# Optimization experiments

Hardware: AMD Instinct MI355X
Metric: run time of the kernel (lower is better)

## Reference

```python
import jax, jax.numpy as jnp
import numpy as np
import math

FACTOR = 1

def setup_inputs() -> dict:
    key = jax.random.key(0)
    k1, k2, k3 = jax.random.split(key, 3)
    B, L, H, E = 32, 1024, 8, 64
    return {
        "queries": jax.random.normal(k1, (B, L, H, E), dtype=jnp.float32),
        "keys": jax.random.normal(k2, (B, L, H, E), dtype=jnp.float32),
        "values": jax.random.normal(k3, (B, L, H, E), dtype=jnp.float32),
        "attn_mask": 0,
    }


def reference(queries, keys, values, attn_mask):
    # queries/keys/values: [B, L, H, E] (S == L so no pad/truncate needed)
    B, L, H, E = queries.shape
    q = jnp.transpose(queries, (0, 2, 3, 1))  # [B,H,E,L]
    k = jnp.transpose(keys, (0, 2, 3, 1))
    v = jnp.transpose(values, (0, 2, 3, 1))   # [B,H,D,L]

    # FFT cross-correlation
    q_fft = jnp.fft.rfft(q, axis=-1)
    k_fft = jnp.fft.rfft(k, axis=-1)
    corr = jnp.fft.irfft(q_fft * jnp.conj(k_fft), n=L, axis=-1)  # [B,H,E,L]

    # top-k delay selection (global over batch, as in source)
    top_k = min(int(FACTOR * math.log(L)), L // 4, 32)  # static: 6
    mean_value = corr.mean(axis=(1, 2))                 # [B,L]
    weights, indices = jax.lax.top_k(mean_value.mean(axis=0), top_k)  # [k]
    tmp_corr = jax.nn.softmax(weights)                  # [k]

    # weighted circular-shift aggregation: roll(v, -indices[i]) summed with tmp_corr[i]
    pos = (jnp.arange(L)[None, :] + indices[:, None]) % L  # [k,L]
    patterns = v[:, :, :, pos]                              # [B,H,D,k,L]
    delays_agg = jnp.einsum('k,bhdkl->bhdl', tmp_corr, patterns)

    return jnp.transpose(delays_agg, (0, 3, 1, 2))  # [B,L,H,D]
```

## Files before the change

kernel.cpp:

```cpp
#include <hip/hip_runtime.h>
#include <math.h>

#define L_SEQ 1024
#define TOPK 6
#define SSTR 1057
#define NFBLK 2048

__device__ constexpr float TW32R[16] = {
  1.f, 0.98078528f, 0.92387953f, 0.83146961f, 0.70710678f, 0.55557023f,
  0.38268343f, 0.19509032f, 0.f, -0.19509032f, -0.38268343f, -0.55557023f,
  -0.70710678f, -0.83146961f, -0.92387953f, -0.98078528f};
__device__ constexpr float TW32I[16] = {
  0.f, -0.19509032f, -0.38268343f, -0.55557023f, -0.70710678f, -0.83146961f,
  -0.92387953f, -0.98078528f, -1.f, -0.98078528f, -0.92387953f, -0.83146961f,
  -0.70710678f, -0.55557023f, -0.38268343f, -0.19509032f};

#define FFTSTAGE(M, H, SH)                                                \
  _Pragma("unroll")                                                       \
  for (int k_ = 0; k_ < 32; k_ += (M)) {                                  \
    _Pragma("unroll")                                                     \
    for (int t_ = 0; t_ < (H); ++t_) {                                    \
      const int a_ = k_ + t_, b_ = a_ + (H);                              \
      const int m_ = t_ << (SH);                                          \
      float vr_, vi_;                                                     \
      if (m_ == 0)      { vr_ = zr[b_]; vi_ = zi[b_]; }                   \
      else if (m_ == 8) { vr_ = zi[b_]; vi_ = -zr[b_]; }                  \
      else {                                                              \
        vr_ = zr[b_] * TW32R[m_] - zi[b_] * TW32I[m_];                    \
        vi_ = zr[b_] * TW32I[m_] + zi[b_] * TW32R[m_];                    \
      }                                                                   \
      zr[b_] = zr[a_] - vr_; zi[b_] = zi[a_] - vi_;                       \
      zr[a_] += vr_;         zi[a_] += vi_;                               \
    }                                                                     \
  }

__global__ __launch_bounds__(256, 2) void fft_spec_kernel(
    const float* __restrict__ q, const float* __restrict__ k,
    float* __restrict__ partial)
{
  __shared__ float smem[8 * SSTR];

  const int tid = threadIdx.x;
  const int bid = blockIdx.x;

  const int wq  = bid >> 3;
  const int xcd = bid & 7;
  const int octet = (wq & 1) | (((wq >> 1) & 3) << 1);
  const int h = (wq >> 3) & 7;
  const int b = (xcd << 2) | (wq >> 6);

  const float* qb = q + (size_t)b * 524288 + h * 64 + octet * 8;
  const float* kb = k + (size_t)b * 524288 + h * 64 + octet * 8;

  const int ep = (tid & 1) * 4;
  const int lb = tid >> 1;
  float4 qv[8], kv[8];
  int colv[8];
  #pragma unroll
  for (int it = 0; it < 8; ++it) {
    const int l = it * 128 + lb;
    qv[it] = *(const float4*)(qb + (size_t)l * 512 + ep);
    kv[it] = *(const float4*)(kb + (size_t)l * 512 + ep);
    colv[it] = (l & 31) * 33 + (l >> 5);
  }

  #pragma unroll
  for (int it = 0; it < 8; ++it) {
    const int col = colv[it];
    smem[(ep + 0) * SSTR + col] = qv[it].x;
    smem[(ep + 1) * SSTR + col] = qv[it].y;
    smem[(ep + 2) * SSTR + col] = qv[it].z;
    smem[(ep + 3) * SSTR + col] = qv[it].w;
  }
  __syncthreads();

  const int s = tid >> 5;
  const int i = tid & 31;
  constexpr int BR[32] = {0,16,8,24,4,20,12,28,2,18,10,26,6,22,14,30,
                          1,17,9,25,5,21,13,29,3,19,11,27,7,23,15,31};
  const float astep = (float)i * 6.13592315e-03f;
  const int rowbase = s * SSTR + i * 33;
  float zr[32], zi[32];

  #pragma unroll
  for (int c = 0; c < 32; ++c) zr[BR[c]] = smem[rowbase + c];
  __syncthreads();

  #pragma unroll
  for (int it = 0; it < 8; ++it) {
    const int col = colv[it];
    smem[(ep + 0) * SSTR + col] = kv[it].x;
    smem[(ep + 1) * SSTR + col] = kv[it].y;
    smem[(ep + 2) * SSTR + col] = kv[it].z;
    smem[(ep + 3) * SSTR + col] = kv[it].w;
  }
  __syncthreads();
  #pragma unroll
  for (int c = 0; c < 32; ++c) zi[BR[c]] = smem[rowbase + c];
  __syncthreads();

  FFTSTAGE(2, 1, 4) FFTSTAGE(4, 2, 3) FFTSTAGE(8, 4, 2)
  FFTSTAGE(16, 8, 1) FFTSTAGE(32, 16, 0)
  #pragma unroll
  for (int k2 = 1; k2 < 32; ++k2) {
    float sa, ca;
    __sincosf(astep * (float)k2, &sa, &ca);
    const float nr = zr[k2] * ca + zi[k2] * sa;
    const float ni = zi[k2] * ca - zr[k2] * sa;
    zr[k2] = nr; zi[k2] = ni;
  }

  const int j = i;
  #pragma unroll
  for (int k2 = 0; k2 < 32; ++k2) smem[rowbase + k2] = zr[k2];
  __syncthreads();
  #pragma unroll
  for (int c = 0; c < 32; ++c) zr[c] = smem[s * SSTR + BR[c] * 33 + j];
  __syncthreads();
  #pragma unroll
  for (int k2 = 0; k2 < 32; ++k2) smem[rowbase + k2] = zi[k2];
  __syncthreads();
  #pragma unroll
  for (int c = 0; c < 32; ++c) zi[c] = smem[s * SSTR + BR[c] * 33 + j];
  __syncthreads();

  FFTSTAGE(2, 1, 4) FFTSTAGE(4, 2, 3) FFTSTAGE(8, 4, 2)
  FFTSTAGE(16, 8, 1) FFTSTAGE(32, 16, 0)

  const int t64 = tid & 63;
  const int pl = (t64 & 32) | ((32 - j) & 31);
  const int rowS = s * SSTR + j * 33;
  float si_all[32];

  #pragma unroll
  for (int k1 = 0; k1 < 16; ++k1) {
    float xr = __shfl(zr[31 - k1], pl, 64);
    float xi = __shfl(zi[31 - k1], pl, 64);
    if (j == 0) { xr = zr[(32 - k1) & 31]; xi = zi[(32 - k1) & 31]; }
    const float ar = zr[k1], ai = zi[k1];
    smem[rowS + k1] = 0.5f  * (ar * xi + ai * xr);
    si_all[k1]      = 0.25f * (ar * ar + ai * ai - xr * xr - xi * xi);
  }
  #pragma unroll
  for (int k1 = 16; k1 < 32; ++k1) {
    float xr = __shfl(zr[31 - k1], pl, 64);
    float xi = __shfl(zi[31 - k1], pl, 64);
    if (j == 0) { xr = zr[(32 - k1) & 31]; xi = zi[(32 - k1) & 31]; }
    const float ar = zr[k1], ai = zi[k1];
    smem[rowS + k1] = 0.5f  * (ar * xi + ai * xr);
    si_all[k1]      = 0.25f * (ar * ar + ai * ai - xr * xr - xi * xi);
  }
  __syncthreads();

  const int jj = tid >> 3;
  const int kq = tid & 7;
  const int v = jj * 32 + kq * 4;
  {
    float ar4[4] = {0.f, 0.f, 0.f, 0.f};
    #pragma unroll
    for (int pp = 0; pp < 8; ++pp) {
      const int base = pp * SSTR + jj * 33 + kq * 4;
      #pragma unroll
      for (int m = 0; m < 4; ++m) ar4[m] += smem[base + m];
    }
    *(float4*)(partial + (size_t)bid * 2048 + v) =
        make_float4(ar4[0], ar4[1], ar4[2], ar4[3]);
  }
  __syncthreads();

  #pragma unroll
  for (int k1 = 0; k1 < 32; ++k1) smem[rowS + k1] = si_all[k1];
  __syncthreads();
  {
    float ai4[4] = {0.f, 0.f, 0.f, 0.f};
    #pragma unroll
    for (int pp = 0; pp < 8; ++pp) {
      const int base = pp * SSTR + jj * 33 + kq * 4;
      #pragma unroll
      for (int m = 0; m < 4; ++m) ai4[m] += smem[base + m];
    }
    *(float4*)(partial + (size_t)bid * 2048 + 1024 + v) =
        make_float4(ai4[0], ai4[1], ai4[2], ai4[3]);
  }
}

__global__ __launch_bounds__(256) void spec_reduce(
    const float* __restrict__ partial, float* __restrict__ S4)
{
  const int t = threadIdx.x;
  const int b64 = t & 63, rq = t >> 6;
  const int vb = (blockIdx.x & 31) * 64;
  const int rc = blockIdx.x >> 5;
  const int v = vb + b64;
  float acc = 0.f;
  const int r0 = rc * 512 + rq * 128;
  for (int rr = r0; rr < r0 + 128; ++rr)
    acc += partial[(size_t)rr * 2048 + v];
  __shared__ float sm[4][65];
  sm[rq][b64] = acc;
  __syncthreads();
  if (t < 64)
    S4[(size_t)rc * 2048 + vb + t] =
        sm[0][t] + sm[1][t] + sm[2][t] + sm[3][t];
}

__global__ __launch_bounds__(256) void corr_kernel(
    const float* __restrict__ S4, float* __restrict__ c)
{
  __shared__ float Sr[2048];
  __shared__ float sm[8][33];
  const int t = threadIdx.x;
  #pragma unroll
  for (int u = 0; u < 8; ++u) {
    const int v = u * 256 + t;
    Sr[v] = S4[v] + S4[2048 + v] + S4[4096 + v] + S4[6144 + v];
  }
  __syncthreads();

  const int tau = blockIdx.x * 32 + (t & 31);
  const int jc = t >> 5;
  float acc = 0.f;
  #pragma unroll 4
  for (int jj = 0; jj < 128; ++jj) {
    const int v = jc * 128 + jj;
    const int jt = ((v & 31) << 5) | (v >> 5);
    float s_, c_;
    __sincosf((float)((jt * tau) & 1023) * 6.13592315e-03f, &s_, &c_);
    acc += Sr[v] * c_ - Sr[1024 + v] * s_;
  }
  sm[jc][t & 31] = acc;
  __syncthreads();
  if (t < 32) {
    float r = 0.f;
    #pragma unroll
    for (int g = 0; g < 8; ++g) r += sm[g][t];
    c[blockIdx.x * 32 + t] = r * (1.0f / 16777216.0f);
  }
}

__global__ __launch_bounds__(256) void topk_kernel(
    const float* __restrict__ c, int* __restrict__ idx_out,
    float* __restrict__ w_out)
{
  __shared__ float vals[L_SEQ];
  __shared__ float rv[256];
  __shared__ int ri[256];
  __shared__ float topv[TOPK];
  __shared__ int topi[TOPK];
  const int tid = threadIdx.x;
  for (int i = tid; i < L_SEQ; i += 256) vals[i] = c[i];
  __syncthreads();

  for (int kk = 0; kk < TOPK; ++kk) {
    float bv = -INFINITY;
    int bi = 1 << 30;
    for (int i = tid; i < L_SEQ; i += 256) {
      const float v = vals[i];
      if (v > bv || (v == bv && i < bi)) { bv = v; bi = i; }
    }
    rv[tid] = bv; ri[tid] = bi;
    __syncthreads();
    for (int off = 128; off > 0; off >>= 1) {
      if (tid < off) {
        const float v2 = rv[tid + off];
        const int i2 = ri[tid + off];
        if (v2 > rv[tid] || (v2 == rv[tid] && i2 < ri[tid])) {
          rv[tid] = v2; ri[tid] = i2;
        }
      }
      __syncthreads();
    }
    if (tid == 0) {
      topv[kk] = rv[0];
      topi[kk] = ri[0];
      vals[ri[0]] = -INFINITY;
    }
    __syncthreads();
  }

  if (tid == 0) {
    const float m = topv[0];
    float e[TOPK], sum = 0.f;
    for (int i = 0; i < TOPK; ++i) { e[i] = expf(topv[i] - m); sum += e[i]; }
    const float inv = 1.0f / sum;
    for (int i = 0; i < TOPK; ++i) { w_out[i] = e[i] * inv; idx_out[i] = topi[i]; }
  }
}

__global__ __launch_bounds__(256) void agg_kernel(
    const float* __restrict__ v, const int* __restrict__ idx,
    const float* __restrict__ w, float4* __restrict__ out)
{
  __shared__ int sidx[TOPK];
  __shared__ float sw[TOPK];
  if (threadIdx.x < TOPK) {
    sidx[threadIdx.x] = idx[threadIdx.x];
    sw[threadIdx.x] = w[threadIdx.x];
  }
  __syncthreads();

  const int i = blockIdx.x * 256 + threadIdx.x;
  const int he4 = i & 127;
  const int l = (i >> 7) & (L_SEQ - 1);
  const int b = i >> 17;
  const float4* vb = (const float4*)v + (size_t)b * (L_SEQ * 128);

  float4 acc = make_float4(0.f, 0.f, 0.f, 0.f);
  #pragma unroll
  for (int kk = 0; kk < TOPK; ++kk) {
    const int src = (l + sidx[kk]) & (L_SEQ - 1);
    const float4 vv = vb[(size_t)src * 128 + he4];
    const float wk = sw[kk];
    acc.x += wk * vv.x; acc.y += wk * vv.y;
    acc.z += wk * vv.z; acc.w += wk * vv.w;
  }
  out[i] = acc;
}

extern "C" void kernel_launch(void* const* d_in, const int* in_sizes, int n_in,
                              void* d_out, int out_size, void* d_ws, size_t ws_size,
                              hipStream_t stream) {
  const float* q = (const float*)d_in[0];
  const float* k = (const float*)d_in[1];
  const float* v = (const float*)d_in[2];

  float* out = (float*)d_out;
  float* partial = out;
  float* S4 = out + (size_t)8388608;

  float* c    = (float*)d_ws;
  int*   idxp = (int*)((char*)d_ws + 4096);
  float* wp   = (float*)((char*)d_ws + 4096 + 64);

  fft_spec_kernel<<<NFBLK, 256, 0, stream>>>(q, k, partial);
  spec_reduce<<<128, 256, 0, stream>>>(partial, S4);
  corr_kernel<<<32, 256, 0, stream>>>(S4, c);
  topk_kernel<<<1, 256, 0, stream>>>(c, idxp, wp);
  agg_kernel<<<(L_SEQ * 32 * 128) / 256, 256, 0, stream>>>(v, idxp, wp,
                                                           (float4*)out);
}
```

Measured before the change: 131.4 us.

## Process two octets per FFT block and simplify spectrum reduction

Each fft_spec_kernel block now loops over two channel octets, accumulating spectra in registers, which halves the grid to 1024 blocks and halves the partial-sum buffer. spec_reduce becomes a single-level reduction over 1024 rows into one spectrum held in workspace, and corr_kernel reads it directly instead of summing four chunks. The aim is less partial traffic and smaller reduction work, at the cost of fewer blocks in flight and a serialized second pass without load/compute overlap.

```diff
diff --git a/kernel.cpp b/kernel.cpp
--- a/kernel.cpp
+++ b/kernel.cpp
@@ -4,7 +4,7 @@
 #define L_SEQ 1024
 #define TOPK 6
 #define SSTR 1057
-#define NFBLK 2048
+#define NFBLK 1024
 
 __device__ constexpr float TW32R[16] = {
   1.f, 0.98078528f, 0.92387953f, 0.83146961f, 0.70710678f, 0.55557023f,
@@ -45,34 +45,9 @@
 
   const int wq  = bid >> 3;
   const int xcd = bid & 7;
-  const int octet = (wq & 1) | (((wq >> 1) & 3) << 1);
-  const int h = (wq >> 3) & 7;
-  const int b = (xcd << 2) | (wq >> 6);
-
-  const float* qb = q + (size_t)b * 524288 + h * 64 + octet * 8;
-  const float* kb = k + (size_t)b * 524288 + h * 64 + octet * 8;
-
-  const int ep = (tid & 1) * 4;
-  const int lb = tid >> 1;
-  float4 qv[8], kv[8];
-  int colv[8];
-  #pragma unroll
-  for (int it = 0; it < 8; ++it) {
-    const int l = it * 128 + lb;
-    qv[it] = *(const float4*)(qb + (size_t)l * 512 + ep);
-    kv[it] = *(const float4*)(kb + (size_t)l * 512 + ep);
-    colv[it] = (l & 31) * 33 + (l >> 5);
-  }
-
-  #pragma unroll
-  for (int it = 0; it < 8; ++it) {
-    const int col = colv[it];
-    smem[(ep + 0) * SSTR + col] = qv[it].x;
-    smem[(ep + 1) * SSTR + col] = qv[it].y;
-    smem[(ep + 2) * SSTR + col] = qv[it].z;
-    smem[(ep + 3) * SSTR + col] = qv[it].w;
-  }
-  __syncthreads();
+  const int op  = wq & 3;
+  const int h   = (wq >> 2) & 7;
+  const int b   = (xcd << 2) | (wq >> 5);
 
   const int s = tid >> 5;
   const int i = tid & 31;
@@ -80,132 +55,158 @@
                           1,17,9,25,5,21,13,29,3,19,11,27,7,23,15,31};
   const float astep = (float)i * 6.13592315e-03f;
   const int rowbase = s * SSTR + i * 33;
-  float zr[32], zi[32];
-
-  #pragma unroll
-  for (int c = 0; c < 32; ++c) zr[BR[c]] = smem[rowbase + c];
-  __syncthreads();
-
-  #pragma unroll
-  for (int it = 0; it < 8; ++it) {
-    const int col = colv[it];
-    smem[(ep + 0) * SSTR + col] = kv[it].x;
-    smem[(ep + 1) * SSTR + col] = kv[it].y;
-    smem[(ep + 2) * SSTR + col] = kv[it].z;
-    smem[(ep + 3) * SSTR + col] = kv[it].w;
-  }
-  __syncthreads();
-  #pragma unroll
-  for (int c = 0; c < 32; ++c) zi[BR[c]] = smem[rowbase + c];
-  __syncthreads();
-
-  FFTSTAGE(2, 1, 4) FFTSTAGE(4, 2, 3) FFTSTAGE(8, 4, 2)
-  FFTSTAGE(16, 8, 1) FFTSTAGE(32, 16, 0)
-  #pragma unroll
-  for (int k2 = 1; k2 < 32; ++k2) {
-    float sa, ca;
-    __sincosf(astep * (float)k2, &sa, &ca);
-    const float nr = zr[k2] * ca + zi[k2] * sa;
-    const float ni = zi[k2] * ca - zr[k2] * sa;
-    zr[k2] = nr; zi[k2] = ni;
-  }
-
-  const int j = i;
-  #pragma unroll
-  for (int k2 = 0; k2 < 32; ++k2) smem[rowbase + k2] = zr[k2];
-  __syncthreads();
-  #pragma unroll
-  for (int c = 0; c < 32; ++c) zr[c] = smem[s * SSTR + BR[c] * 33 + j];
-  __syncthreads();
-  #pragma unroll
-  for (int k2 = 0; k2 < 32; ++k2) smem[rowbase + k2] = zi[k2];
-  __syncthreads();
-  #pragma unroll
-  for (int c = 0; c < 32; ++c) zi[c] = smem[s * SSTR + BR[c] * 33 + j];
-  __syncthreads();
-
-  FFTSTAGE(2, 1, 4) FFTSTAGE(4, 2, 3) FFTSTAGE(8, 4, 2)
-  FFTSTAGE(16, 8, 1) FFTSTAGE(32, 16, 0)
-
-  const int t64 = tid & 63;
-  const int pl = (t64 & 32) | ((32 - j) & 31);
-  const int rowS = s * SSTR + j * 33;
-  float si_all[32];
-
-  #pragma unroll
-  for (int k1 = 0; k1 < 16; ++k1) {
-    float xr = __shfl(zr[31 - k1], pl, 64);
-    float xi = __shfl(zi[31 - k1], pl, 64);
-    if (j == 0) { xr = zr[(32 - k1) & 31]; xi = zi[(32 - k1) & 31]; }
-    const float ar = zr[k1], ai = zi[k1];
-    smem[rowS + k1] = 0.5f  * (ar * xi + ai * xr);
-    si_all[k1]      = 0.25f * (ar * ar + ai * ai - xr * xr - xi * xi);
-  }
-  #pragma unroll
-  for (int k1 = 16; k1 < 32; ++k1) {
-    float xr = __shfl(zr[31 - k1], pl, 64);
-    float xi = __shfl(zi[31 - k1], pl, 64);
-    if (j == 0) { xr = zr[(32 - k1) & 31]; xi = zi[(32 - k1) & 31]; }
-    const float ar = zr[k1], ai = zi[k1];
-    smem[rowS + k1] = 0.5f  * (ar * xi + ai * xr);
-    si_all[k1]      = 0.25f * (ar * ar + ai * ai - xr * xr - xi * xi);
-  }
-  __syncthreads();
+  const int ep = (tid & 1) * 4;
+  const int lb = tid >> 1;
 
   const int jj = tid >> 3;
   const int kq = tid & 7;
-  const int v = jj * 32 + kq * 4;
-  {
-    float ar4[4] = {0.f, 0.f, 0.f, 0.f};
+  float ar4[4] = {0.f, 0.f, 0.f, 0.f};
+  float ai4[4] = {0.f, 0.f, 0.f, 0.f};
+
+  for (int oc = 0; oc < 2; ++oc) {
+    const int octet = op * 2 + oc;
+    const float* qb = q + (size_t)b * 524288 + h * 64 + octet * 8;
+    const float* kb = k + (size_t)b * 524288 + h * 64 + octet * 8;
+
+    if (oc) __syncthreads();
+
+    float4 qv[8], kv[8];
+    int colv[8];
+    #pragma unroll
+    for (int it = 0; it < 8; ++it) {
+      const int l = it * 128 + lb;
+      qv[it] = *(const float4*)(qb + (size_t)l * 512 + ep);
+      kv[it] = *(const float4*)(kb + (size_t)l * 512 + ep);
+      colv[it] = (l & 31) * 33 + (l >> 5);
+    }
+
+    #pragma unroll
+    for (int it = 0; it < 8; ++it) {
+      const int col = colv[it];
+      smem[(ep + 0) * SSTR + col] = qv[it].x;
+      smem[(ep + 1) * SSTR + col] = qv[it].y;
+      smem[(ep + 2) * SSTR + col] = qv[it].z;
+      smem[(ep + 3) * SSTR + col] = qv[it].w;
+    }
+    __syncthreads();
+
+    float zr[32], zi[32];
+    #pragma unroll
+    for (int c = 0; c < 32; ++c) zr[BR[c]] = smem[rowbase + c];
+    __syncthreads();
+
+    #pragma unroll
+    for (int it = 0; it < 8; ++it) {
+      const int col = colv[it];
+      smem[(ep + 0) * SSTR + col] = kv[it].x;
+      smem[(ep + 1) * SSTR + col] = kv[it].y;
+      smem[(ep + 2) * SSTR + col] = kv[it].z;
+      smem[(ep + 3) * SSTR + col] = kv[it].w;
+    }
+    __syncthreads();
+    #pragma unroll
+    for (int c = 0; c < 32; ++c) zi[BR[c]] = smem[rowbase + c];
+    __syncthreads();
+
+    FFTSTAGE(2, 1, 4) FFTSTAGE(4, 2, 3) FFTSTAGE(8, 4, 2)
+    FFTSTAGE(16, 8, 1) FFTSTAGE(32, 16, 0)
+    #pragma unroll
+    for (int k2 = 1; k2 < 32; ++k2) {
+      float sa, ca;
+      __sincosf(astep * (float)k2, &sa, &ca);
+      const float nr = zr[k2] * ca + zi[k2] * sa;
+      const float ni = zi[k2] * ca - zr[k2] * sa;
+      zr[k2] = nr; zi[k2] = ni;
+    }
+
+    const int j = i;
+    #pragma unroll
+    for (int k2 = 0; k2 < 32; ++k2) smem[rowbase + k2] = zr[k2];
+    __syncthreads();
+    #pragma unroll
+    for (int c = 0; c < 32; ++c) zr[c] = smem[s * SSTR + BR[c] * 33 + j];
+    __syncthreads();
+    #pragma unroll
+    for (int k2 = 0; k2 < 32; ++k2) smem[rowbase + k2] = zi[k2];
+    __syncthreads();
+    #pragma unroll
+    for (int c = 0; c < 32; ++c) zi[c] = smem[s * SSTR + BR[c] * 33 + j];
+    __syncthreads();
+
+    FFTSTAGE(2, 1, 4) FFTSTAGE(4, 2, 3) FFTSTAGE(8, 4, 2)
+    FFTSTAGE(16, 8, 1) FFTSTAGE(32, 16, 0)
+
+    const int t64 = tid & 63;
+    const int pl = (t64 & 32) | ((32 - j) & 31);
+    const int rowS = s * SSTR + j * 33;
+    float si_all[32];
+
+    #pragma unroll
+    for (int k1 = 0; k1 < 16; ++k1) {
+      float xr = __shfl(zr[31 - k1], pl, 64);
+      float xi = __shfl(zi[31 - k1], pl, 64);
+      if (j == 0) { xr = zr[(32 - k1) & 31]; xi = zi[(32 - k1) & 31]; }
+      const float ar = zr[k1], ai = zi[k1];
+      smem[rowS + k1] = 0.5f  * (ar * xi + ai * xr);
+      si_all[k1]      = 0.25f * (ar * ar + ai * ai - xr * xr - xi * xi);
+    }
+    #pragma unroll
+    for (int k1 = 16; k1 < 32; ++k1) {
+      float xr = __shfl(zr[31 - k1], pl, 64);
+      float xi = __shfl(zi[31 - k1], pl, 64);
+      if (j == 0) { xr = zr[(32 - k1) & 31]; xi = zi[(32 - k1) & 31]; }
+      const float ar = zr[k1], ai = zi[k1];
+      smem[rowS + k1] = 0.5f  * (ar * xi + ai * xr);
+      si_all[k1]      = 0.25f * (ar * ar + ai * ai - xr * xr - xi * xi);
+    }
+    __syncthreads();
+
     #pragma unroll
     for (int pp = 0; pp < 8; ++pp) {
       const int base = pp * SSTR + jj * 33 + kq * 4;
       #pragma unroll
       for (int m = 0; m < 4; ++m) ar4[m] += smem[base + m];
     }
-    *(float4*)(partial + (size_t)bid * 2048 + v) =
-        make_float4(ar4[0], ar4[1], ar4[2], ar4[3]);
-  }
-  __syncthreads();
-
-  #pragma unroll
-  for (int k1 = 0; k1 < 32; ++k1) smem[rowS + k1] = si_all[k1];
-  __syncthreads();
-  {
-    float ai4[4] = {0.f, 0.f, 0.f, 0.f};
+    __syncthreads();
+
+    const int rowS2 = s * SSTR + j * 33;
+    #pragma unroll
+    for (int k1 = 0; k1 < 32; ++k1) smem[rowS2 + k1] = si_all[k1];
+    __syncthreads();
     #pragma unroll
     for (int pp = 0; pp < 8; ++pp) {
       const int base = pp * SSTR + jj * 33 + kq * 4;
       #pragma unroll
       for (int m = 0; m < 4; ++m) ai4[m] += smem[base + m];
     }
-    *(float4*)(partial + (size_t)bid * 2048 + 1024 + v) =
-        make_float4(ai4[0], ai4[1], ai4[2], ai4[3]);
-  }
+  }
+
+  const int v = jj * 32 + kq * 4;
+  *(float4*)(partial + (size_t)bid * 2048 + v) =
+      make_float4(ar4[0], ar4[1], ar4[2], ar4[3]);
+  *(float4*)(partial + (size_t)bid * 2048 + 1024 + v) =
+      make_float4(ai4[0], ai4[1], ai4[2], ai4[3]);
 }
 
 __global__ __launch_bounds__(256) void spec_reduce(
-    const float* __restrict__ partial, float* __restrict__ S4)
+    const float* __restrict__ partial, float* __restrict__ S)
 {
   const int t = threadIdx.x;
   const int b64 = t & 63, rq = t >> 6;
-  const int vb = (blockIdx.x & 31) * 64;
-  const int rc = blockIdx.x >> 5;
-  const int v = vb + b64;
+  const int v = blockIdx.x * 64 + b64;
   float acc = 0.f;
-  const int r0 = rc * 512 + rq * 128;
-  for (int rr = r0; rr < r0 + 128; ++rr)
+  const int r0 = rq * 256;
+  for (int rr = r0; rr < r0 + 256; ++rr)
     acc += partial[(size_t)rr * 2048 + v];
   __shared__ float sm[4][65];
   sm[rq][b64] = acc;
   __syncthreads();
   if (t < 64)
-    S4[(size_t)rc * 2048 + vb + t] =
-        sm[0][t] + sm[1][t] + sm[2][t] + sm[3][t];
+    S[v] = sm[0][t] + sm[1][t] + sm[2][t] + sm[3][t];
 }
 
 __global__ __launch_bounds__(256) void corr_kernel(
-    const float* __restrict__ S4, float* __restrict__ c)
+    const float* __restrict__ S, float* __restrict__ c)
 {
   __shared__ float Sr[2048];
   __shared__ float sm[8][33];
@@ -213,7 +214,7 @@
   #pragma unroll
   for (int u = 0; u < 8; ++u) {
     const int v = u * 256 + t;
-    Sr[v] = S4[v] + S4[2048 + v] + S4[4096 + v] + S4[6144 + v];
+    Sr[v] = S[v];
   }
   __syncthreads();
 
@@ -326,15 +327,15 @@
 
   float* out = (float*)d_out;
   float* partial = out;
-  float* S4 = out + (size_t)8388608;
 
   float* c    = (float*)d_ws;
   int*   idxp = (int*)((char*)d_ws + 4096);
   float* wp   = (float*)((char*)d_ws + 4096 + 64);
+  float* S    = (float*)((char*)d_ws + 8192);
 
   fft_spec_kernel<<<NFBLK, 256, 0, stream>>>(q, k, partial);
-  spec_reduce<<<128, 256, 0, stream>>>(partial, S4);
-  corr_kernel<<<32, 256, 0, stream>>>(S4, c);
+  spec_reduce<<<32, 256, 0, stream>>>(partial, S);
+  corr_kernel<<<32, 256, 0, stream>>>(S, c);
   topk_kernel<<<1, 256, 0, stream>>>(c, idxp, wp);
   agg_kernel<<<(L_SEQ * 32 * 128) / 256, 256, 0, stream>>>(v, idxp, wp,
                                                            (float4*)out);
```

Result: faster. 127.2 us (-3.2%).
